# Optimization experiments

Hardware: AMD Instinct MI355X
Metric: run time of the kernel (lower is better)

The kernel has to match this reference:

```python
import jax, jax.numpy as jnp
import numpy as np

T, B, E, H = 1024, 4, 1024, 16


def setup_inputs() -> dict:
    key0 = jax.random.key(0)
    ks = jax.random.split(key0, 10)
    query = jax.random.normal(ks[0], (T, B, E), jnp.float32)
    key_t = jax.random.normal(ks[1], (T, B, E), jnp.float32)
    # causal additive mask [T, T] (0 on/below diagonal, -inf above)
    causal = jnp.where(jnp.tril(jnp.ones((T, T), bool)), 0.0, -jnp.inf).astype(jnp.float32)
    # per-row valid lengths in [T//2, T]; True = padded key position
    lengths = jax.random.randint(ks[2], (B,), T // 2, T + 1)
    key_padding_mask = jnp.arange(T)[None, :] >= lengths[:, None]  # [B, T] bool
    scale = E ** -0.5
    Wq = jax.random.normal(ks[3], (E, E), jnp.float32) * scale
    Wk = jax.random.normal(ks[4], (E, E), jnp.float32) * scale
    Wv = jax.random.normal(ks[5], (E, E), jnp.float32) * scale
    bq = jax.random.normal(ks[6], (E,), jnp.float32) * 0.02
    bk = jax.random.normal(ks[7], (E,), jnp.float32) * 0.02
    bv = jax.random.normal(ks[8], (E,), jnp.float32) * 0.02
    return dict(query=query, key=key_t, key_padding_mask=key_padding_mask,
                attn_mask=causal, Wq=Wq, bq=bq, Wk=Wk, bk=bk, Wv=Wv, bv=bv,
                num_heads=H)


def reference(query, key, key_padding_mask, attn_mask, Wq, bq, Wk, bk, Wv, bv, num_heads):
    # Self-attention path (encoder_decoder_attention=False, layer_state=None):
    # k, v computed from `query`; `key` is unused (matches torch forward).
    t, b, e = query.shape
    h = num_heads
    d = e // h
    scaling = d ** -0.5
    q = (query @ Wq.T + bq) * scaling          # [T, B, E]
    k = query @ Wk.T + bk
    v = query @ Wv.T + bv

    def _shape(x):  # [T, B, E] -> [B*H, T, D]
        return x.reshape(t, b * h, d).transpose(1, 0, 2)

    q, k, v = _shape(q), _shape(k), _shape(v)
    attn = jnp.einsum('ztd,zsd->zts', q, k)    # [B*H, T, S]
    attn = attn.reshape(b, h, t, t) + attn_mask            # additive causal mask
    attn = jnp.where(key_padding_mask[:, None, None, :], -jnp.inf, attn)
    probs = jax.nn.softmax(attn, axis=-1)                   # dropout p=0.0
    out = jnp.einsum('bhts,bhsd->bhtd', probs, v.reshape(b, h, t, d))
    # [B,H,T,D] -> [B*H,T,D] -> [T,B*H,D] -> [T,B,E]
    out = out.reshape(b * h, t, d).transpose(1, 0, 2).reshape(t, b, e)
    return out
```

## Files before the change

### kernel.cpp

```cpp
#include <hip/hip_runtime.h>
#include <cstdint>


typedef __attribute__((ext_vector_type(8))) short short8;
typedef __attribute__((ext_vector_type(4))) float floatx4;
typedef __attribute__((ext_vector_type(16))) float floatx16;
typedef __attribute__((ext_vector_type(4))) unsigned short u16x4;
typedef unsigned short u16;

#define T_DIM 1024
#define B_DIM 4
#define E_DIM 1024
#define H_DIM 16
#define D_DIM 64
#define M_DIM (T_DIM * B_DIM)
#define N_DIM (3 * E_DIM)
#define K_DIM E_DIM
#define KT_NUM (K_DIM / 64)

__device__ __forceinline__ u16 f2bf(float f) {
  uint32_t u = __builtin_bit_cast(uint32_t, f);
  u += 0x7fffu + ((u >> 16) & 1u);
  return (u16)(u >> 16);
}

__device__ __forceinline__ void gload_lds16(const void* g, void* l) {
  __builtin_amdgcn_global_load_lds(
      (const __attribute__((address_space(1))) uint32_t*)g,
      (__attribute__((address_space(3))) uint32_t*)l, 16, 0, 0);
}

__device__ __forceinline__ uint32_t swz(uint32_t row, uint32_t cb) {
  return row * 128u + (cb ^ ((row & 7u) << 4));
}

#define BARRIER()  __builtin_amdgcn_s_barrier()
#define WAIT_VM6   asm volatile("s_waitcnt vmcnt(6)" ::: "memory")
#define WAIT_VM0   asm volatile("s_waitcnt vmcnt(0)" ::: "memory")

__global__ __launch_bounds__(256) void convert_k(
    const float* __restrict__ q, const float* __restrict__ wq,
    const float* __restrict__ wk, const float* __restrict__ wv,
    u16* __restrict__ Abf, u16* __restrict__ Wbf,
    const int* __restrict__ kpm, int* __restrict__ lengths) {
  if (blockIdx.x >= 7168) {
    __shared__ int cnt;
    if (threadIdx.x == 0) cnt = 0;
    __syncthreads();
    int b = blockIdx.x - 7168;
    int local = 0;
    for (int t = threadIdx.x; t < T_DIM; t += 256)
      local += (kpm[b * T_DIM + t] == 0) ? 1 : 0;
    atomicAdd(&cnt, local);
    __syncthreads();
    if (threadIdx.x == 0) lengths[b] = cnt;
    return;
  }
  size_t i = ((size_t)blockIdx.x * 256 + threadIdx.x) * 4;
  const float* src;
  u16* dst;
  if (i < (size_t)M_DIM * K_DIM) {
    src = q + i;
    dst = Abf + i;
  } else {
    size_t off = i - (size_t)M_DIM * K_DIM;
    int x = (int)(off >> 20);
    size_t within = off & 1048575u;
    src = (x == 0 ? wq : (x == 1 ? wk : wv)) + within;
    dst = Wbf + off;
  }
  float4 v = *(const float4*)src;
  u16x4 o;
  o.x = f2bf(v.x); o.y = f2bf(v.y); o.z = f2bf(v.z); o.w = f2bf(v.w);
  *(u16x4*)dst = o;
}

__global__ __launch_bounds__(512, 2) void qkv_gemm(
    const u16* __restrict__ A, const u16* __restrict__ W,
    const float* __restrict__ bq, const float* __restrict__ bk,
    const float* __restrict__ bv,
    u16* __restrict__ qo, u16* __restrict__ ko, u16* __restrict__ vto) {
  __shared__ alignas(16) char lds[131072];
  const int tid = threadIdx.x;
  const int lane = tid & 63, w = tid >> 6;
  const int fr = lane & 15, fg = lane >> 4;
  const int wm = (w >> 2) * 64, wn = (w & 3) * 96;
  const int srow = lane >> 3;
  const int scol = ((lane & 7) ^ srow) * 16;

  const int bid = blockIdx.x;
  const int n0 = (bid & 7) * 384;
  const int m0 = (bid >> 3) * 128;

  floatx4 acc[4][6] = {};
  short8 af[4][2];
  short8 bfr[6][2];

  auto stage = [&](int kt, int g) {
    if (kt >= KT_NUM) return;
    char* buf = lds + (kt & 1) * 65536;
#pragma unroll
    for (int it = 0; it < 2; ++it) {
      int mrow = it * 64 + w * 8 + srow;
      if (g == 0) {
        int gr = m0 + mrow;
        int ga = (gr & 1023) * 4 + (gr >> 10);
        gload_lds16((const char*)A + (size_t)ga * 2048 + kt * 128 + scol,
                    buf + mrow * 128);
      } else {
        int r = 16 * (3 * (mrow >> 4) + (g - 1)) + (mrow & 15);
        gload_lds16((const char*)W + (size_t)(n0 + r) * 2048 + kt * 128 + scol,
                    buf + 16384 + r * 128);
      }
    }
  };
  auto read_a = [&](const char* buf) {
#pragma unroll
    for (int i = 0; i < 4; ++i)
#pragma unroll
      for (int kk = 0; kk < 2; ++kk)
        af[i][kk] = *(const short8*)(buf + swz(wm + i * 16 + fr, kk * 64 + fg * 16));
  };
  auto read_b = [&](const char* buf, int j0) {
#pragma unroll
    for (int jj = 0; jj < 2; ++jj) {
      int j = j0 + jj * 3;
#pragma unroll
      for (int kk = 0; kk < 2; ++kk)
        bfr[j][kk] = *(const short8*)(buf + 16384 +
                                      swz(wn + j * 16 + fr, kk * 64 + fg * 16));
    }
  };
  auto mfma_pair = [&](int j0) {
    __builtin_amdgcn_s_setprio(1);
#pragma unroll
    for (int kk = 0; kk < 2; ++kk)
#pragma unroll
      for (int i = 0; i < 4; ++i)
#pragma unroll
        for (int jj = 0; jj < 2; ++jj) {
          int j = j0 + jj * 3;
          acc[i][j] = __builtin_amdgcn_mfma_f32_16x16x32_bf16(
              af[i][kk], bfr[j][kk], acc[i][j], 0, 0, 0);
        }
    __builtin_amdgcn_s_setprio(0);
  };

  stage(0, 0); stage(0, 1); stage(0, 2); stage(0, 3);
  stage(1, 0); stage(1, 1); stage(1, 2);
  WAIT_VM6;
  BARRIER();

  const char* buf0 = lds;
  const char* buf1 = lds + 65536;

  for (int i = 0; i < KT_NUM / 2; ++i) {
    const int t = 2 * i;
    const bool last = (i == KT_NUM / 2 - 1);
    read_a(buf0);
    read_b(buf0, 0);
    stage(t + 1, 3);
    BARRIER();
    mfma_pair(0);
    BARRIER();
    read_b(buf0, 1);
    stage(t + 2, 0);
    stage(t + 2, 1);
    BARRIER();
    mfma_pair(1);
    BARRIER();
    read_b(buf0, 2);
    stage(t + 2, 2);
    BARRIER();
    mfma_pair(2);
    if (last) { WAIT_VM0; } else { WAIT_VM6; }
    BARRIER();
    read_a(buf1);
    read_b(buf1, 0);
    stage(t + 2, 3);
    BARRIER();
    mfma_pair(0);
    BARRIER();
    read_b(buf1, 1);
    stage(t + 3, 0);
    stage(t + 3, 1);
    BARRIER();
    mfma_pair(1);
    BARRIER();
    read_b(buf1, 2);
    stage(t + 3, 2);
    BARRIER();
    mfma_pair(2);
    if (!last) WAIT_VM6;
    BARRIER();
  }

#pragma unroll
  for (int j = 0; j < 6; ++j) {
    int col = n0 + wn + j * 16 + fr;
    int x = col >> 10;
    int within = col & 1023;
    int h = within >> 6, d = within & 63;
    float bias = (x == 0) ? bq[within] : ((x == 1) ? bk[within] : bv[within]);
    float scale = (x == 0) ? 0.125f * 1.44269504f : 1.0f;
#pragma unroll
    for (int i = 0; i < 4; ++i) {
      int mp = m0 + wm + i * 16 + fg * 4;
      int b = mp >> 10, t0 = mp & 1023;
      int z = b * H_DIM + h;
      if (x == 2) {
        u16x4 pk;
#pragma unroll
        for (int r = 0; r < 4; ++r)
          pk[r] = f2bf(acc[i][j][r] + bias);
        *(u16x4*)(vto + (size_t)(z * D_DIM + d) * T_DIM + t0) = pk;
      } else {
        u16* dstp = (x == 0) ? qo : ko;
#pragma unroll
        for (int r = 0; r < 4; ++r)
          dstp[((size_t)z * T_DIM + t0 + r) * D_DIM + d] =
              f2bf((acc[i][j][r] + bias) * scale);
      }
    }
  }
}

__global__ __launch_bounds__(256) void attn_k(
    const u16* __restrict__ qbuf, const u16* __restrict__ kbuf,
    const u16* __restrict__ vtb, const int* __restrict__ lengths,
    float* __restrict__ out) {
  __shared__ alignas(16) char Klds[2][128 * 128];
  __shared__ alignas(16) char Vlds[2][128 * 128];

  const int bid = blockIdx.x;
  const int xcd = bid & 7, idx = bid >> 3;
  const int z = (idx & 7) * 8 + xcd;
  const int qb = 7 - (idx >> 3);
  const int b = z >> 4, h = z & 15;
  const int tid = threadIdx.x, lane = tid & 63, w = tid >> 6;
  const int l31 = lane & 31, hi = lane >> 5;
  const int srow = lane >> 3;
  const int scol = ((lane & 7) ^ srow) * 16;

  const int length = lengths[b];
  const int t0 = qb * 128;
  const int t0w = t0 + w * 32;
  const int t = t0w + l31;
  const int s_hi = min(t0 + 128, length);
  const int n_tiles = (s_hi + 127) >> 7;

  short8 qf[4];
#pragma unroll
  for (int dk = 0; dk < 4; ++dk)
    qf[dk] = *(const short8*)(qbuf + ((size_t)z * T_DIM + t) * D_DIM + dk * 16 + hi * 8);

  floatx16 accT[2] = {};
  float m = -1e30f, lsum = 0.f;

  auto stageKV = [&](int st, int buf) {
    const int s0 = st * 128;
#pragma unroll
    for (int it = 0; it < 4; ++it) {
      int rb = w * 32 + it * 8;
      gload_lds16((const char*)kbuf + ((size_t)z * T_DIM + s0 + rb + srow) * 128 + scol,
                  Klds[buf] + rb * 128);
      gload_lds16((const char*)vtb + ((size_t)(z * D_DIM + (rb & 63) + srow)) * 2048 +
                      s0 * 2 + (rb >> 6) * 128 + scol,
                  Vlds[buf] + rb * 128);
    }
  };

  stageKV(0, 0);
  __syncthreads();
  int cur = 0;

  for (int st = 0; st < n_tiles; ++st) {
    const int s0 = st * 128;
    if (st + 1 < n_tiles) stageKV(st + 1, cur ^ 1);

    if (s0 <= t0w + 31) {
      floatx16 sT[4] = {};
      __builtin_amdgcn_s_setprio(1);
#pragma unroll
      for (int sh = 0; sh < 4; ++sh)
#pragma unroll
        for (int dk = 0; dk < 4; ++dk) {
          short8 kf = *(const short8*)(Klds[cur] + swz(sh * 32 + l31, dk * 32 + hi * 16));
          sT[sh] = __builtin_amdgcn_mfma_f32_32x32x16_bf16(kf, qf[dk], sT[sh], 0, 0, 0);
        }
      __builtin_amdgcn_s_setprio(0);

      if (s0 + 127 > t0w || s0 + 127 >= length) {
#pragma unroll
        for (int sh = 0; sh < 4; ++sh)
#pragma unroll
          for (int r = 0; r < 16; ++r) {
            int s = s0 + sh * 32 + (r & 3) + 8 * (r >> 2) + 4 * hi;
            if (s > t || s >= length) sT[sh][r] = -1e30f;
          }
      }

      float tmax = -1e30f;
#pragma unroll
      for (int sh = 0; sh < 4; ++sh)
#pragma unroll
        for (int r = 0; r < 16; ++r) tmax = fmaxf(tmax, sT[sh][r]);
      tmax = fmaxf(tmax, __shfl_xor(tmax, 32, 64));
      if (!__all(tmax <= m + 8.0f)) {
        float mn = fmaxf(m, tmax);
        float corr = __builtin_exp2f(m - mn);
        m = mn;
        lsum *= corr;
#pragma unroll
        for (int dh = 0; dh < 2; ++dh)
#pragma unroll
          for (int r = 0; r < 16; ++r) accT[dh][r] *= corr;
      }
      float rs = 0.f;
#pragma unroll
      for (int sh = 0; sh < 4; ++sh)
#pragma unroll
        for (int r = 0; r < 16; ++r) {
          float p = __builtin_exp2f(sT[sh][r] - m);
          sT[sh][r] = p;
          rs += p;
        }
      lsum += rs;

#pragma unroll
      for (int sh = 0; sh < 4; ++sh) {
        uint32_t a[8];
#pragma unroll
        for (int i = 0; i < 8; ++i)
          asm("v_cvt_pk_bf16_f32 %0, %1, %2"
              : "=v"(a[i]) : "v"(sT[sh][2 * i]), "v"(sT[sh][2 * i + 1]));
        uint32_t oth[8];
#pragma unroll
        for (int i = 0; i < 8; ++i)
          oth[i] = (uint32_t)__shfl_xor((int)a[i], 32, 64);
        short8 pa[2];
#pragma unroll
        for (int q = 0; q < 2; ++q) {
          union { uint32_t u[4]; short8 v; } pk;
          pk.u[0] = hi ? oth[4 * q + 2] : a[4 * q + 0];
          pk.u[1] = hi ? oth[4 * q + 3] : a[4 * q + 1];
          pk.u[2] = hi ? a[4 * q + 2] : oth[4 * q + 0];
          pk.u[3] = hi ? a[4 * q + 3] : oth[4 * q + 1];
          pa[q] = pk.v;
        }
        __builtin_amdgcn_s_setprio(1);
#pragma unroll
        for (int dh = 0; dh < 2; ++dh)
#pragma unroll
          for (int q = 0; q < 2; ++q) {
            int ks = sh * 2 + q;
            int sub = ks >> 2, ksw = ks & 3;
            short8 vf = *(const short8*)(Vlds[cur] +
                swz(sub * 64 + dh * 32 + l31, ksw * 32 + hi * 16));
            accT[dh] = __builtin_amdgcn_mfma_f32_32x32x16_bf16(vf, pa[q], accT[dh], 0, 0, 0);
          }
        __builtin_amdgcn_s_setprio(0);
      }
    }

    __syncthreads();
    cur ^= 1;
  }

  lsum += __shfl_xor(lsum, 32, 64);
  float inv = 1.0f / lsum;
#pragma unroll
  for (int dh = 0; dh < 2; ++dh)
#pragma unroll
    for (int q = 0; q < 4; ++q) {
      float4 o4;
      o4.x = accT[dh][4 * q + 0] * inv;
      o4.y = accT[dh][4 * q + 1] * inv;
      o4.z = accT[dh][4 * q + 2] * inv;
      o4.w = accT[dh][4 * q + 3] * inv;
      int d = 8 * q + 4 * hi + 32 * dh;
      *(float4*)(out + (size_t)t * (B_DIM * E_DIM) + b * E_DIM + h * D_DIM + d) = o4;
    }
}

extern "C" void kernel_launch(void* const* d_in, const int* in_sizes, int n_in,
                              void* d_out, int out_size, void* d_ws, size_t ws_size,
                              hipStream_t stream) {
  const float* query = (const float*)d_in[0];
  const int* kpm = (const int*)d_in[2];
  const float* Wq = (const float*)d_in[4];
  const float* bq = (const float*)d_in[5];
  const float* Wk = (const float*)d_in[6];
  const float* bk = (const float*)d_in[7];
  const float* Wv = (const float*)d_in[8];
  const float* bv = (const float*)d_in[9];

  char* ws = (char*)d_ws;
  u16* Abf = (u16*)ws;
  u16* Wbf = (u16*)(ws + 8388608);
  u16* qb_ = (u16*)(ws + 14680064);
  u16* kb_ = (u16*)(ws + 23068672);
  u16* vtb = (u16*)(ws + 31457280);
  int* lengths = (int*)(ws + 39845888);

  convert_k<<<7172, 256, 0, stream>>>(query, Wq, Wk, Wv, Abf, Wbf, kpm, lengths);
  qkv_gemm<<<256, 512, 0, stream>>>(Abf, Wbf, bq, bk, bv, qb_, kb_, vtb);
  attn_k<<<512, 256, 0, stream>>>(qb_, kb_, vtb, lengths, (float*)d_out);
}
```

Measured before the change: 76.46 us.

## Switch QKV GEMM to 32x32 MFMA and skip fully-masked attention subtiles

The QKV projection GEMM moves from 16x16x32 MFMA tiles to 32x32x16 MFMA tiles, changing the accumulator layout, fragment loads and epilogue indexing. The goal is fewer LDS fragment reads and MFMA instructions per K step. In attention, the causal skip now works per 32-row key subtile rather than per 128-row tile, so fully masked subtiles avoid QK MFMAs, masking, exp and PV work. The trade-off is more divergent control flow, and a higher chance of register pressure from the larger floatx16 accumulators.

Result: slower. 86.93 us (+13.7%).

```diff
diff --git a/kernel.cpp b/kernel.cpp
--- a/kernel.cpp
+++ b/kernel.cpp
@@ -3,7 +3,6 @@
 
 
 typedef __attribute__((ext_vector_type(8))) short short8;
-typedef __attribute__((ext_vector_type(4))) float floatx4;
 typedef __attribute__((ext_vector_type(16))) float floatx16;
 typedef __attribute__((ext_vector_type(4))) unsigned short u16x4;
 typedef unsigned short u16;
@@ -83,7 +82,7 @@
   __shared__ alignas(16) char lds[131072];
   const int tid = threadIdx.x;
   const int lane = tid & 63, w = tid >> 6;
-  const int fr = lane & 15, fg = lane >> 4;
+  const int l31 = lane & 31, hi = lane >> 5;
   const int wm = (w >> 2) * 64, wn = (w & 3) * 96;
   const int srow = lane >> 3;
   const int scol = ((lane & 7) ^ srow) * 16;
@@ -92,9 +91,9 @@
   const int n0 = (bid & 7) * 384;
   const int m0 = (bid >> 3) * 128;
 
-  floatx4 acc[4][6] = {};
-  short8 af[4][2];
-  short8 bfr[6][2];
+  floatx16 acc[2][3] = {};
+  short8 af[2][4];
+  short8 bfr[4];
 
   auto stage = [&](int kt, int g) {
     if (kt >= KT_NUM) return;
@@ -108,7 +107,7 @@
         gload_lds16((const char*)A + (size_t)ga * 2048 + kt * 128 + scol,
                     buf + mrow * 128);
       } else {
-        int r = 16 * (3 * (mrow >> 4) + (g - 1)) + (mrow & 15);
+        int r = 32 * (3 * (mrow >> 5) + (g - 1)) + (mrow & 31);
         gload_lds16((const char*)W + (size_t)(n0 + r) * 2048 + kt * 128 + scol,
                     buf + 16384 + r * 128);
       }
@@ -116,33 +115,25 @@
   };
   auto read_a = [&](const char* buf) {
 #pragma unroll
-    for (int i = 0; i < 4; ++i)
-#pragma unroll
-      for (int kk = 0; kk < 2; ++kk)
-        af[i][kk] = *(const short8*)(buf + swz(wm + i * 16 + fr, kk * 64 + fg * 16));
+    for (int mb = 0; mb < 2; ++mb)
+#pragma unroll
+      for (int kk = 0; kk < 4; ++kk)
+        af[mb][kk] = *(const short8*)(buf + swz(wm + mb * 32 + l31, kk * 32 + hi * 16));
   };
-  auto read_b = [&](const char* buf, int j0) {
-#pragma unroll
-    for (int jj = 0; jj < 2; ++jj) {
-      int j = j0 + jj * 3;
-#pragma unroll
-      for (int kk = 0; kk < 2; ++kk)
-        bfr[j][kk] = *(const short8*)(buf + 16384 +
-                                      swz(wn + j * 16 + fr, kk * 64 + fg * 16));
-    }
+  auto read_b = [&](const char* buf, int jb) {
+#pragma unroll
+    for (int kk = 0; kk < 4; ++kk)
+      bfr[kk] = *(const short8*)(buf + 16384 +
+                                 swz(wn + jb * 32 + l31, kk * 32 + hi * 16));
   };
-  auto mfma_pair = [&](int j0) {
+  auto mfma_blk = [&](int jb) {
     __builtin_amdgcn_s_setprio(1);
 #pragma unroll
-    for (int kk = 0; kk < 2; ++kk)
-#pragma unroll
-      for (int i = 0; i < 4; ++i)
-#pragma unroll
-        for (int jj = 0; jj < 2; ++jj) {
-          int j = j0 + jj * 3;
-          acc[i][j] = __builtin_amdgcn_mfma_f32_16x16x32_bf16(
-              af[i][kk], bfr[j][kk], acc[i][j], 0, 0, 0);
-        }
+    for (int kk = 0; kk < 4; ++kk)
+#pragma unroll
+      for (int mb = 0; mb < 2; ++mb)
+        acc[mb][jb] = __builtin_amdgcn_mfma_f32_32x32x16_bf16(
+            af[mb][kk], bfr[kk], acc[mb][jb], 0, 0, 0);
     __builtin_amdgcn_s_setprio(0);
   };
 
@@ -161,65 +152,68 @@
     read_b(buf0, 0);
     stage(t + 1, 3);
     BARRIER();
-    mfma_pair(0);
+    mfma_blk(0);
     BARRIER();
     read_b(buf0, 1);
     stage(t + 2, 0);
     stage(t + 2, 1);
     BARRIER();
-    mfma_pair(1);
+    mfma_blk(1);
     BARRIER();
     read_b(buf0, 2);
     stage(t + 2, 2);
     BARRIER();
-    mfma_pair(2);
+    mfma_blk(2);
     if (last) { WAIT_VM0; } else { WAIT_VM6; }
     BARRIER();
     read_a(buf1);
     read_b(buf1, 0);
     stage(t + 2, 3);
     BARRIER();
-    mfma_pair(0);
+    mfma_blk(0);
     BARRIER();
     read_b(buf1, 1);
     stage(t + 3, 0);
     stage(t + 3, 1);
     BARRIER();
-    mfma_pair(1);
+    mfma_blk(1);
     BARRIER();
     read_b(buf1, 2);
     stage(t + 3, 2);
     BARRIER();
-    mfma_pair(2);
+    mfma_blk(2);
     if (!last) WAIT_VM6;
     BARRIER();
   }
 
 #pragma unroll
-  for (int j = 0; j < 6; ++j) {
-    int col = n0 + wn + j * 16 + fr;
+  for (int jb = 0; jb < 3; ++jb) {
+    int col = n0 + wn + jb * 32 + l31;
     int x = col >> 10;
     int within = col & 1023;
     int h = within >> 6, d = within & 63;
     float bias = (x == 0) ? bq[within] : ((x == 1) ? bk[within] : bv[within]);
     float scale = (x == 0) ? 0.125f * 1.44269504f : 1.0f;
 #pragma unroll
-    for (int i = 0; i < 4; ++i) {
-      int mp = m0 + wm + i * 16 + fg * 4;
-      int b = mp >> 10, t0 = mp & 1023;
-      int z = b * H_DIM + h;
-      if (x == 2) {
-        u16x4 pk;
-#pragma unroll
-        for (int r = 0; r < 4; ++r)
-          pk[r] = f2bf(acc[i][j][r] + bias);
-        *(u16x4*)(vto + (size_t)(z * D_DIM + d) * T_DIM + t0) = pk;
-      } else {
-        u16* dstp = (x == 0) ? qo : ko;
-#pragma unroll
-        for (int r = 0; r < 4; ++r)
-          dstp[((size_t)z * T_DIM + t0 + r) * D_DIM + d] =
-              f2bf((acc[i][j][r] + bias) * scale);
+    for (int mb = 0; mb < 2; ++mb) {
+#pragma unroll
+      for (int qd = 0; qd < 4; ++qd) {
+        int mp = m0 + wm + mb * 32 + 8 * qd + 4 * hi;
+        int b = mp >> 10, t0 = mp & 1023;
+        int z = b * H_DIM + h;
+        if (x == 2) {
+          u16x4 pk;
+#pragma unroll
+          for (int r = 0; r < 4; ++r)
+            pk[r] = f2bf(acc[mb][jb][4 * qd + r] + bias);
+          *(u16x4*)(vto + (size_t)(z * D_DIM + d) * T_DIM + t0) = pk;
+        } else {
+          u16* dstp = (x == 0) ? qo : ko;
+#pragma unroll
+          for (int r = 0; r < 4; ++r)
+            dstp[((size_t)z * T_DIM + t0 + r) * D_DIM + d] =
+                f2bf((acc[mb][jb][4 * qd + r] + bias) * scale);
+        }
       }
     }
   }
@@ -278,33 +272,36 @@
     const int s0 = st * 128;
     if (st + 1 < n_tiles) stageKV(st + 1, cur ^ 1);
 
-    if (s0 <= t0w + 31) {
+    {
       floatx16 sT[4] = {};
       __builtin_amdgcn_s_setprio(1);
 #pragma unroll
       for (int sh = 0; sh < 4; ++sh)
-#pragma unroll
-        for (int dk = 0; dk < 4; ++dk) {
-          short8 kf = *(const short8*)(Klds[cur] + swz(sh * 32 + l31, dk * 32 + hi * 16));
-          sT[sh] = __builtin_amdgcn_mfma_f32_32x32x16_bf16(kf, qf[dk], sT[sh], 0, 0, 0);
-        }
+        if (s0 + sh * 32 <= t0w + 31)
+#pragma unroll
+          for (int dk = 0; dk < 4; ++dk) {
+            short8 kf = *(const short8*)(Klds[cur] + swz(sh * 32 + l31, dk * 32 + hi * 16));
+            sT[sh] = __builtin_amdgcn_mfma_f32_32x32x16_bf16(kf, qf[dk], sT[sh], 0, 0, 0);
+          }
       __builtin_amdgcn_s_setprio(0);
 
       if (s0 + 127 > t0w || s0 + 127 >= length) {
 #pragma unroll
         for (int sh = 0; sh < 4; ++sh)
-#pragma unroll
-          for (int r = 0; r < 16; ++r) {
-            int s = s0 + sh * 32 + (r & 3) + 8 * (r >> 2) + 4 * hi;
-            if (s > t || s >= length) sT[sh][r] = -1e30f;
-          }
+          if (s0 + sh * 32 <= t0w + 31)
+#pragma unroll
+            for (int r = 0; r < 16; ++r) {
+              int s = s0 + sh * 32 + (r & 3) + 8 * (r >> 2) + 4 * hi;
+              if (s > t || s >= length) sT[sh][r] = -1e30f;
+            }
       }
 
       float tmax = -1e30f;
 #pragma unroll
       for (int sh = 0; sh < 4; ++sh)
-#pragma unroll
-        for (int r = 0; r < 16; ++r) tmax = fmaxf(tmax, sT[sh][r]);
+        if (s0 + sh * 32 <= t0w + 31)
+#pragma unroll
+          for (int r = 0; r < 16; ++r) tmax = fmaxf(tmax, sT[sh][r]);
       tmax = fmaxf(tmax, __shfl_xor(tmax, 32, 64));
       if (!__all(tmax <= m + 8.0f)) {
         float mn = fmaxf(m, tmax);
@@ -319,16 +316,18 @@
       float rs = 0.f;
 #pragma unroll
       for (int sh = 0; sh < 4; ++sh)
-#pragma unroll
-        for (int r = 0; r < 16; ++r) {
-          float p = __builtin_exp2f(sT[sh][r] - m);
-          sT[sh][r] = p;
-          rs += p;
-        }
+        if (s0 + sh * 32 <= t0w + 31)
+#pragma unroll
+          for (int r = 0; r < 16; ++r) {
+            float p = __builtin_exp2f(sT[sh][r] - m);
+            sT[sh][r] = p;
+            rs += p;
+          }
       lsum += rs;
 
 #pragma unroll
       for (int sh = 0; sh < 4; ++sh) {
+        if (s0 + sh * 32 > t0w + 31) continue;
         uint32_t a[8];
 #pragma unroll
         for (int i = 0; i < 8; ++i)
```

## Split KV tiles across two wave groups in attention and merge partial softmax

Applied to the files above, without the earlier changes.

The attention block doubles from 4 to 8 waves. The two halves of the block take alternating 128-wide KV tiles for the same 128 query rows, which shortens each wave's serial loop over tiles. At the end, the upper half writes its running max, sum and accumulators to shared memory, and the lower half rescales and merges them before normalising and storing. This adds a merge step, an extra barrier and more register pressure under the 512-thread launch bound. Each staged tile is now consumed by only half the waves.

After: 80.91 us. 5.8% more time.

```diff
diff --git a/kernel.cpp b/kernel.cpp
--- a/kernel.cpp
+++ b/kernel.cpp
@@ -225,12 +225,11 @@
   }
 }
 
-__global__ __launch_bounds__(256) void attn_k(
+__global__ __launch_bounds__(512) void attn_k(
     const u16* __restrict__ qbuf, const u16* __restrict__ kbuf,
     const u16* __restrict__ vtb, const int* __restrict__ lengths,
     float* __restrict__ out) {
-  __shared__ alignas(16) char Klds[2][128 * 128];
-  __shared__ alignas(16) char Vlds[2][128 * 128];
+  __shared__ alignas(16) char smem[65536];
 
   const int bid = blockIdx.x;
   const int xcd = bid & 7, idx = bid >> 3;
@@ -239,16 +238,22 @@
   const int b = z >> 4, h = z & 15;
   const int tid = threadIdx.x, lane = tid & 63, w = tid >> 6;
   const int l31 = lane & 31, hi = lane >> 5;
+  const int sparity = w >> 2;
   const int srow = lane >> 3;
   const int scol = ((lane & 7) ^ srow) * 16;
 
   const int length = lengths[b];
   const int t0 = qb * 128;
-  const int t0w = t0 + w * 32;
+  const int t0w = t0 + (w & 3) * 32;
   const int t = t0w + l31;
   const int s_hi = min(t0 + 128, length);
   const int n_tiles = (s_hi + 127) >> 7;
 
+  char* Kb0 = smem;
+  char* Kb1 = smem + 16384;
+  char* Vb0 = smem + 32768;
+  char* Vb1 = smem + 49152;
+
   short8 qf[4];
 #pragma unroll
   for (int dk = 0; dk < 4; ++dk)
@@ -259,14 +264,16 @@
 
   auto stageKV = [&](int st, int buf) {
     const int s0 = st * 128;
-#pragma unroll
-    for (int it = 0; it < 4; ++it) {
-      int rb = w * 32 + it * 8;
+    char* Kd = buf ? Kb1 : Kb0;
+    char* Vd = buf ? Vb1 : Vb0;
+#pragma unroll
+    for (int it = 0; it < 2; ++it) {
+      int rb = w * 16 + it * 8;
       gload_lds16((const char*)kbuf + ((size_t)z * T_DIM + s0 + rb + srow) * 128 + scol,
-                  Klds[buf] + rb * 128);
+                  Kd + rb * 128);
       gload_lds16((const char*)vtb + ((size_t)(z * D_DIM + (rb & 63) + srow)) * 2048 +
                       s0 * 2 + (rb >> 6) * 128 + scol,
-                  Vlds[buf] + rb * 128);
+                  Vd + rb * 128);
     }
   };
 
@@ -278,14 +285,16 @@
     const int s0 = st * 128;
     if (st + 1 < n_tiles) stageKV(st + 1, cur ^ 1);
 
-    if (s0 <= t0w + 31) {
+    if (((st & 1) == sparity) && (s0 <= t0w + 31)) {
+      const char* Kc = cur ? Kb1 : Kb0;
+      const char* Vc = cur ? Vb1 : Vb0;
       floatx16 sT[4] = {};
       __builtin_amdgcn_s_setprio(1);
 #pragma unroll
       for (int sh = 0; sh < 4; ++sh)
 #pragma unroll
         for (int dk = 0; dk < 4; ++dk) {
-          short8 kf = *(const short8*)(Klds[cur] + swz(sh * 32 + l31, dk * 32 + hi * 16));
+          short8 kf = *(const short8*)(Kc + swz(sh * 32 + l31, dk * 32 + hi * 16));
           sT[sh] = __builtin_amdgcn_mfma_f32_32x32x16_bf16(kf, qf[dk], sT[sh], 0, 0, 0);
         }
       __builtin_amdgcn_s_setprio(0);
@@ -355,7 +364,7 @@
           for (int q = 0; q < 2; ++q) {
             int ks = sh * 2 + q;
             int sub = ks >> 2, ksw = ks & 3;
-            short8 vf = *(const short8*)(Vlds[cur] +
+            short8 vf = *(const short8*)(Vc +
                 swz(sub * 64 + dh * 32 + l31, ksw * 32 + hi * 16));
             accT[dh] = __builtin_amdgcn_mfma_f32_32x32x16_bf16(vf, pa[q], accT[dh], 0, 0, 0);
           }
@@ -367,20 +376,46 @@
     cur ^= 1;
   }
 
-  lsum += __shfl_xor(lsum, 32, 64);
-  float inv = 1.0f / lsum;
-#pragma unroll
-  for (int dh = 0; dh < 2; ++dh)
-#pragma unroll
-    for (int q = 0; q < 4; ++q) {
-      float4 o4;
-      o4.x = accT[dh][4 * q + 0] * inv;
-      o4.y = accT[dh][4 * q + 1] * inv;
-      o4.z = accT[dh][4 * q + 2] * inv;
-      o4.w = accT[dh][4 * q + 3] * inv;
-      int d = 8 * q + 4 * hi + 32 * dh;
-      *(float4*)(out + (size_t)t * (B_DIM * E_DIM) + b * E_DIM + h * D_DIM + d) = o4;
-    }
+  float* mrg = (float*)smem;
+  if (w >= 4) {
+    int base = ((w - 4) * 64 + lane) * 34;
+    mrg[base] = m;
+    mrg[base + 1] = lsum;
+#pragma unroll
+    for (int dh = 0; dh < 2; ++dh)
+#pragma unroll
+      for (int r = 0; r < 16; ++r)
+        mrg[base + 2 + dh * 16 + r] = accT[dh][r];
+  }
+  __syncthreads();
+  if (w < 4) {
+    int base = (w * 64 + lane) * 34;
+    float mb = mrg[base], lb = mrg[base + 1];
+    float M = fmaxf(m, mb);
+    float wa = __builtin_exp2f(m - M);
+    float wb = __builtin_exp2f(mb - M);
+    lsum = wa * lsum + wb * lb;
+#pragma unroll
+    for (int dh = 0; dh < 2; ++dh)
+#pragma unroll
+      for (int r = 0; r < 16; ++r)
+        accT[dh][r] = wa * accT[dh][r] + wb * mrg[base + 2 + dh * 16 + r];
+
+    lsum += __shfl_xor(lsum, 32, 64);
+    float inv = 1.0f / lsum;
+#pragma unroll
+    for (int dh = 0; dh < 2; ++dh)
+#pragma unroll
+      for (int q = 0; q < 4; ++q) {
+        float4 o4;
+        o4.x = accT[dh][4 * q + 0] * inv;
+        o4.y = accT[dh][4 * q + 1] * inv;
+        o4.z = accT[dh][4 * q + 2] * inv;
+        o4.w = accT[dh][4 * q + 3] * inv;
+        int d = 8 * q + 4 * hi + 32 * dh;
+        *(float4*)(out + (size_t)t * (B_DIM * E_DIM) + b * E_DIM + h * D_DIM + d) = o4;
+      }
+  }
 }
 
 extern "C" void kernel_launch(void* const* d_in, const int* in_sizes, int n_in,
@@ -405,5 +440,5 @@
 
   convert_k<<<7172, 256, 0, stream>>>(query, Wq, Wk, Wv, Abf, Wbf, kpm, lengths);
   qkv_gemm<<<256, 512, 0, stream>>>(Abf, Wbf, bq, bk, bv, qb_, kb_, vtb);
-  attn_k<<<512, 256, 0, stream>>>(qb_, kb_, vtb, lengths, (float*)d_out);
-}
+  attn_k<<<512, 512, 0, stream>>>(qb_, kb_, vtb, lengths, (float*)d_out);
+}
```
